# Kernel optimization log

Measured on AMD Instinct MI355X. Metric: run time of the kernel, lower is better.

## Reference

```python
import jax, jax.numpy as jnp
import numpy as np

N = 50000
E = 800000
IN_DIM = 128
HID = 128
OUT = 40


def setup_inputs() -> dict:
    key = jax.random.key(0)
    k1, k2, k3, k4, k5 = jax.random.split(key, 5)
    x = jax.random.normal(k1, (N, IN_DIM), dtype=jnp.float32)
    edge_index = jax.random.randint(k2, (2, E), 0, N, dtype=jnp.int64)
    # Glorot-ish init for GCNConv weights, zero bias (PyG default bias=True)
    W1 = jax.random.normal(k3, (IN_DIM, HID), dtype=jnp.float32) / np.sqrt(IN_DIM)
    b1 = jnp.zeros((HID,), dtype=jnp.float32)
    W2 = jax.random.normal(k4, (HID, OUT), dtype=jnp.float32) / np.sqrt(HID)
    b2 = jnp.zeros((OUT,), dtype=jnp.float32)
    return {"x": x, "edge_index": edge_index, "W1": W1, "b1": b1, "W2": W2, "b2": b2}


def _gcn_norm(edge_index, n_nodes):
    """Add self-loops and compute symmetric GCN normalization per edge.
    Returns (src, dst, norm) with len E + n_nodes."""
    loops = jnp.arange(n_nodes, dtype=edge_index.dtype)
    src = jnp.concatenate([edge_index[0], loops])
    dst = jnpp_concat = jnp.concatenate([edge_index[1], loops])
    dst = jnp.concatenate([edge_index[1], loops])
    deg = jax.ops.segment_sum(jnp.ones_like(dst, dtype=jnp.float32), dst,
                              num_segments=n_nodes)
    dinv = jnp.where(deg > 0, jax.lax.rsqrt(deg), 0.0)
    norm = dinv[src] * dinv[dst]  # [E + N]
    return src, dst, norm


def _gcn_conv(x, src, dst, norm, W, b, n_nodes):
    xw = x @ W                                  # [N, F_out] transform first
    msg = xw[src] * norm[:, None]               # gather + scale, [E+N, F_out]
    out = jax.ops.segment_sum(msg, dst, num_segments=n_nodes)  # scatter-add
    return out + b


def reference(x, edge_index, W1, b1, W2, b2):
    n = x.shape[0]
    src, dst, norm = _gcn_norm(edge_index, n)
    h = _gcn_conv(x, src, dst, norm, W1, b1, n)
    h = jax.nn.relu(h)
    # dropout is identity in eval mode (training=False)
    h = _gcn_conv(h, src, dst, norm, W2, b2, n)
    return jax.nn.softmax(h, axis=1)
```

## Files before the change

### kernel.cpp

```cpp
#include <hip/hip_runtime.h>
#include <hip/hip_fp16.h>

#define IN_DIM 128
#define HID    128
#define OUTC   40
#define CAP    64
#define LSTR   136
#define NBS    1024

typedef _Float16 f16x8 __attribute__((ext_vector_type(8)));
typedef _Float16 f16x4 __attribute__((ext_vector_type(4)));
typedef float    f32x4 __attribute__((ext_vector_type(4)));
typedef int      i32x4 __attribute__((ext_vector_type(4)));

__device__ __forceinline__ int permi(int d, int NP8) { return (d & 7) * NP8 + (d >> 3); }

__device__ __forceinline__ f16x8 cvt8(f32x4 lo, f32x4 hi) {
  f16x8 r;
  r[0] = (_Float16)lo[0]; r[1] = (_Float16)lo[1]; r[2] = (_Float16)lo[2]; r[3] = (_Float16)lo[3];
  r[4] = (_Float16)hi[0]; r[5] = (_Float16)hi[1]; r[6] = (_Float16)hi[2]; r[7] = (_Float16)hi[3];
  return r;
}

__global__ __launch_bounds__(256) void k_scatter(const int* __restrict__ edge, int* __restrict__ cnt,
                                                 unsigned short* __restrict__ col,
                                                 int E, int n, int NP8) {
  int b = blockIdx.x, tid = threadIdx.x;
  int g = b & 7;
  int E4 = E >> 2;
  auto proc = [&](int d, int s) {
    if ((d & 7) != g || (unsigned)d >= (unsigned)n || (unsigned)s >= (unsigned)n) return;
    int p   = g * NP8 + (d >> 3);
    int pos = atomicAdd(&cnt[p], 1);
    if (pos < CAP) col[(size_t)p * CAP + pos] = (unsigned short)s;
  };
  int j = b >> 3;
  int t = j * 256 + tid;
  const int gstride = (NBS >> 3) * 256;
  const i32x4* srcv = (const i32x4*)edge;
  const i32x4* dstv = (const i32x4*)&edge[E];
  for (int q = t; q < E4; q += gstride) {
    i32x4 dq = __builtin_nontemporal_load(&dstv[q]);
    i32x4 sq = __builtin_nontemporal_load(&srcv[q]);
    proc(dq[0], sq[0]); proc(dq[1], sq[1]); proc(dq[2], sq[2]); proc(dq[3], sq[3]);
  }
  if (b == 0) {
    for (int e = E4 * 4 + tid; e < E; e += 256) {
      int d  = edge[E + e];
      int sv = edge[e];
      if ((unsigned)d >= (unsigned)n || (unsigned)sv >= (unsigned)n) continue;
      int p   = (d & 7) * NP8 + (d >> 3);
      int pos = atomicAdd(&cnt[p], 1);
      if (pos < CAP) col[(size_t)p * CAP + pos] = (unsigned short)sv;
    }
  }
}

__global__ __launch_bounds__(256) void k_gemm1(const float* __restrict__ x, const float* __restrict__ W1,
                                               const int* __restrict__ cnt, __half* __restrict__ xws,
                                               int n, int NP8) {
  __shared__ _Float16 sW[128 * LSTR];
  int tid = threadIdx.x;
  int i0  = blockIdx.x * 64;

  {
    const f32x4* w4 = (const f32x4*)W1;
    for (int idx = tid; idx < 4096; idx += 256) {
      int kk = idx >> 5, nn4 = (idx & 31) * 4;
      f32x4 v = w4[idx];
      sW[(nn4 + 0) * LSTR + kk] = (_Float16)v[0];
      sW[(nn4 + 1) * LSTR + kk] = (_Float16)v[1];
      sW[(nn4 + 2) * LSTR + kk] = (_Float16)v[2];
      sW[(nn4 + 3) * LSTR + kk] = (_Float16)v[3];
    }
  }
  __syncthreads();

  int wv = tid >> 6, lane = tid & 63, m = lane & 15, quad = lane >> 4;
  int arow = i0 + 16 * wv + m;
  f16x8 a0, a1, a2, a3;
  if (arow < n) {
    const float* xr = &x[(size_t)arow * IN_DIM + quad * 8];
    f32x4 u0 = __builtin_nontemporal_load((const f32x4*)(xr));
    f32x4 u1 = __builtin_nontemporal_load((const f32x4*)(xr + 4));
    f32x4 u2 = __builtin_nontemporal_load((const f32x4*)(xr + 32));
    f32x4 u3 = __builtin_nontemporal_load((const f32x4*)(xr + 36));
    f32x4 u4 = __builtin_nontemporal_load((const f32x4*)(xr + 64));
    f32x4 u5 = __builtin_nontemporal_load((const f32x4*)(xr + 68));
    f32x4 u6 = __builtin_nontemporal_load((const f32x4*)(xr + 96));
    f32x4 u7 = __builtin_nontemporal_load((const f32x4*)(xr + 100));
    a0 = cvt8(u0, u1); a1 = cvt8(u2, u3); a2 = cvt8(u4, u5); a3 = cvt8(u6, u7);
  } else {
#pragma unroll
    for (int jj = 0; jj < 8; ++jj) {
      a0[jj] = (_Float16)0.f; a1[jj] = (_Float16)0.f; a2[jj] = (_Float16)0.f; a3[jj] = (_Float16)0.f;
    }
  }

  int base_row = i0 + 16 * wv + quad * 4;
  float dvr[4];
#pragma unroll
  for (int r = 0; r < 4; ++r) {
    int row = base_row + r;
    dvr[r] = (row < n) ? rsqrtf((float)(cnt[permi(row, NP8)] + 1)) : 0.f;
  }

#pragma unroll
  for (int t = 0; t < 8; ++t) {
    const _Float16* bx = &sW[(t * 16 + m) * LSTR + quad * 8];
    f16x8 bf0 = *(const f16x8*)(bx);
    f16x8 bf1 = *(const f16x8*)(bx + 32);
    f16x8 bf2 = *(const f16x8*)(bx + 64);
    f16x8 bf3 = *(const f16x8*)(bx + 96);
    f32x4 c = {0.f, 0.f, 0.f, 0.f};
    c = __builtin_amdgcn_mfma_f32_16x16x32_f16(a0, bf0, c, 0, 0, 0);
    c = __builtin_amdgcn_mfma_f32_16x16x32_f16(a1, bf1, c, 0, 0, 0);
    c = __builtin_amdgcn_mfma_f32_16x16x32_f16(a2, bf2, c, 0, 0, 0);
    c = __builtin_amdgcn_mfma_f32_16x16x32_f16(a3, bf3, c, 0, 0, 0);
    int colb = t * 16 + m;
#pragma unroll
    for (int r = 0; r < 4; ++r) {
      int row = base_row + r;
      if (row < n) xws[(size_t)row * HID + colb] = __float2half(c[r] * dvr[r]);
    }
  }
}

__global__ __launch_bounds__(256) void k_agg1(const uint2* __restrict__ xws2, const int* __restrict__ cnt,
                                              const unsigned short* __restrict__ col, const float* __restrict__ b1,
                                              uint2* __restrict__ hv, int n, int NP8, int nbHalf) {
  int bi = blockIdx.x, tid = threadIdx.x;
  int ph = 0;
  if (bi >= nbHalf) { ph = 1; bi -= nbHalf; }
  int sub = (tid >> 4) & 3;
  int f16i = tid & 15;
  int wid = bi * 16 + ((tid >> 6) << 2) + sub;
  if (wid >= n) return;
  int fo = ph * 16 + f16i;
  int p   = permi(wid, NP8);
  int deg = cnt[p];
  float dvd = rsqrtf((float)(deg + 1));
  uint2 sv = xws2[(size_t)wid * 32 + fo];
  float2 alo = __half22float2(*(__half2*)&sv.x);
  float2 ahi = __half22float2(*(__half2*)&sv.y);
  float ax = alo.x, ay = alo.y, az = ahi.x, aw = ahi.y;
  int end = min(deg, CAP);
  const unsigned short* cp = &col[(size_t)p * CAP];
  int e = 0;
  for (; e + 4 <= end; e += 4) {
    uint2 cw = *(const uint2*)&cp[e];
    int s0 = cw.x & 0xffff, s1 = cw.x >> 16;
    int s2 = cw.y & 0xffff, s3 = cw.y >> 16;
    uint2 v0 = xws2[(size_t)s0 * 32 + fo];
    uint2 v1 = xws2[(size_t)s1 * 32 + fo];
    uint2 v2 = xws2[(size_t)s2 * 32 + fo];
    uint2 v3 = xws2[(size_t)s3 * 32 + fo];
    float2 l0 = __half22float2(*(__half2*)&v0.x), h0 = __half22float2(*(__half2*)&v0.y);
    float2 l1 = __half22float2(*(__half2*)&v1.x), h1 = __half22float2(*(__half2*)&v1.y);
    float2 l2 = __half22float2(*(__half2*)&v2.x), h2 = __half22float2(*(__half2*)&v2.y);
    float2 l3 = __half22float2(*(__half2*)&v3.x), h3 = __half22float2(*(__half2*)&v3.y);
    ax += (l0.x + l1.x) + (l2.x + l3.x);
    ay += (l0.y + l1.y) + (l2.y + l3.y);
    az += (h0.x + h1.x) + (h2.x + h3.x);
    aw += (h0.y + h1.y) + (h2.y + h3.y);
  }
  for (; e < end; ++e) {
    uint2 v = xws2[(size_t)cp[e] * 32 + fo];
    float2 l = __half22float2(*(__half2*)&v.x), hh = __half22float2(*(__half2*)&v.y);
    ax += l.x; ay += l.y; az += hh.x; aw += hh.y;
  }
  float4 bb = ((const float4*)b1)[fo];
  __half2 o0 = __floats2half2_rn(fmaxf(ax * dvd + bb.x, 0.f), fmaxf(ay * dvd + bb.y, 0.f));
  __half2 o1 = __floats2half2_rn(fmaxf(az * dvd + bb.z, 0.f), fmaxf(aw * dvd + bb.w, 0.f));
  uint2 o; o.x = *(unsigned*)&o0; o.y = *(unsigned*)&o1;
  hv[(size_t)wid * 32 + fo] = o;
}

__global__ __launch_bounds__(256) void k_gemm2(const __half* __restrict__ h, const float* __restrict__ W2,
                                               const int* __restrict__ cnt, __half* __restrict__ out,
                                               int n, int NP8) {
  __shared__ _Float16 sW[48 * LSTR];
  __shared__ _Float16 sH[64 * LSTR];
  int tid = threadIdx.x;
  int i0  = blockIdx.x * 64;

  for (int idx = tid; idx < 8192; idx += 256) {
    int nn = idx & 63, kk = idx >> 6;
    if (nn < 48) sW[nn * LSTR + kk] = (nn < OUTC) ? (_Float16)W2[kk * OUTC + nn] : (_Float16)0.f;
  }
  {
    const uint4* src = (const uint4*)h;
    for (int idx = tid; idx < 1024; idx += 256) {
      int r = idx >> 4, c = idx & 15;
      int row = i0 + r;
      uint4 v = (row < n) ? src[(size_t)row * 16 + c] : make_uint4(0u, 0u, 0u, 0u);
      *(uint4*)&sH[r * LSTR + c * 8] = v;
    }
  }
  __syncthreads();

  int wv = tid >> 6, lane = tid & 63, m = lane & 15, quad = lane >> 4;
  const _Float16* axp = &sH[(16 * wv + m) * LSTR + quad * 8];
  f16x8 a0 = *(const f16x8*)(axp);
  f16x8 a1 = *(const f16x8*)(axp + 32);
  f16x8 a2 = *(const f16x8*)(axp + 64);
  f16x8 a3 = *(const f16x8*)(axp + 96);

  int base_row = i0 + 16 * wv + quad * 4;
  float dvr[4];
#pragma unroll
  for (int r = 0; r < 4; ++r) {
    int row = base_row + r;
    dvr[r] = (row < n) ? rsqrtf((float)(cnt[permi(row, NP8)] + 1)) : 0.f;
  }

#pragma unroll
  for (int t = 0; t < 3; ++t) {
    const _Float16* bx = &sW[(t * 16 + m) * LSTR + quad * 8];
    f16x8 bf0 = *(const f16x8*)(bx);
    f16x8 bf1 = *(const f16x8*)(bx + 32);
    f16x8 bf2 = *(const f16x8*)(bx + 64);
    f16x8 bf3 = *(const f16x8*)(bx + 96);
    f32x4 c = {0.f, 0.f, 0.f, 0.f};
    c = __builtin_amdgcn_mfma_f32_16x16x32_f16(a0, bf0, c, 0, 0, 0);
    c = __builtin_amdgcn_mfma_f32_16x16x32_f16(a1, bf1, c, 0, 0, 0);
    c = __builtin_amdgcn_mfma_f32_16x16x32_f16(a2, bf2, c, 0, 0, 0);
    c = __builtin_amdgcn_mfma_f32_16x16x32_f16(a3, bf3, c, 0, 0, 0);
    int colb = t * 16 + m;
    if (colb < OUTC) {
#pragma unroll
      for (int r = 0; r < 4; ++r) {
        int row = base_row + r;
        if (row < n) out[(size_t)row * OUTC + colb] = __float2half(c[r] * dvr[r]);
      }
    }
  }
}

__global__ __launch_bounds__(256) void k_agg2(const __half2* __restrict__ hw2, const int* __restrict__ cnt,
                                              const unsigned short* __restrict__ col, const float* __restrict__ b2,
                                              float* __restrict__ out, int n, int NP8) {
  int wpair = (blockIdx.x * 256 + threadIdx.x) >> 6;
  int lane  = threadIdx.x & 63;
  int half  = lane >> 5;
  int f     = lane & 31;
  int wid   = wpair * 2 + half;
  bool act  = (f < OUTC / 2) && (wid < n);
  int widc  = (wid < n) ? wid : 0;
  int li    = act ? f : 0;
  int p     = permi(widc, NP8);
  int deg   = (wid < n) ? cnt[p] : 0;
  float2 acc = act ? __half22float2(hw2[(size_t)widc * (OUTC / 2) + li]) : make_float2(0.f, 0.f);
  int end = min(deg, CAP);
  const unsigned short* cp = &col[(size_t)p * CAP];
  int e = 0;
  for (; e + 8 <= end; e += 8) {
    uint4 cw = *(const uint4*)&cp[e];
    int s0 = cw.x & 0xffff, s1 = cw.x >> 16, s2 = cw.y & 0xffff, s3 = cw.y >> 16;
    int s4 = cw.z & 0xffff, s5 = cw.z >> 16, s6 = cw.w & 0xffff, s7 = cw.w >> 16;
    if (act) {
      float2 v0 = __half22float2(hw2[(size_t)s0 * (OUTC / 2) + li]);
      float2 v1 = __half22float2(hw2[(size_t)s1 * (OUTC / 2) + li]);
      float2 v2 = __half22float2(hw2[(size_t)s2 * (OUTC / 2) + li]);
      float2 v3 = __half22float2(hw2[(size_t)s3 * (OUTC / 2) + li]);
      float2 v4 = __half22float2(hw2[(size_t)s4 * (OUTC / 2) + li]);
      float2 v5 = __half22float2(hw2[(size_t)s5 * (OUTC / 2) + li]);
      float2 v6 = __half22float2(hw2[(size_t)s6 * (OUTC / 2) + li]);
      float2 v7 = __half22float2(hw2[(size_t)s7 * (OUTC / 2) + li]);
      acc.x += (v0.x + v1.x) + (v2.x + v3.x) + ((v4.x + v5.x) + (v6.x + v7.x));
      acc.y += (v0.y + v1.y) + (v2.y + v3.y) + ((v4.y + v5.y) + (v6.y + v7.y));
    }
  }
  for (; e < end; ++e) {
    int s = cp[e];
    if (act) {
      float2 v = __half22float2(hw2[(size_t)s * (OUTC / 2) + li]);
      acc.x += v.x; acc.y += v.y;
    }
  }
  float dvd = rsqrtf((float)(deg + 1));
  float2 bb = act ? ((const float2*)b2)[li] : make_float2(0.f, 0.f);
  float lx = act ? acc.x * dvd + bb.x : -1e30f;
  float ly = act ? acc.y * dvd + bb.y : -1e30f;
  float m = fmaxf(lx, ly);
#pragma unroll
  for (int o = 16; o > 0; o >>= 1) m = fmaxf(m, __shfl_xor(m, o, 32));
  float ex = act ? __expf(lx - m) : 0.f;
  float ey = act ? __expf(ly - m) : 0.f;
  float sum = ex + ey;
#pragma unroll
  for (int o = 16; o > 0; o >>= 1) sum += __shfl_xor(sum, o, 32);
  if (act) {
    float inv = 1.f / sum;
    ((float2*)out)[(size_t)wid * (OUTC / 2) + li] = make_float2(ex * inv, ey * inv);
  }
}


extern "C" void kernel_launch(void* const* d_in, const int* in_sizes, int n_in,
                              void* d_out, int out_size, void* d_ws, size_t ws_size,
                              hipStream_t stream) {
  const float* x    = (const float*)d_in[0];
  const int*   edge = (const int*)d_in[1];
  const float* W1   = (const float*)d_in[2];
  const float* b1   = (const float*)d_in[3];
  const float* W2   = (const float*)d_in[4];
  const float* b2   = (const float*)d_in[5];
  float* out = (float*)d_out;

  int N   = in_sizes[0] / IN_DIM;
  int E   = in_sizes[1] / 2;
  int NP8 = (N + 7) / 8;
  int NP  = NP8 * 8;

  char* ws = (char*)d_ws;
  size_t off = 0;
  auto carve = [&](size_t bytes) { char* p = ws + off; off = (off + bytes + 255) & ~(size_t)255; return p; };
  int*            cnt = (int*)carve((size_t)NP * 4);
  unsigned short* col = (unsigned short*)carve((size_t)NP * CAP * 2);
  __half*         xws = (__half*)carve((size_t)N * HID * 2);
  __half*         h   = (__half*)carve((size_t)N * HID * 2);
  __half*         hw  = xws;

  (void)hipMemsetAsync(cnt, 0, (size_t)NP * 4, stream);

  int nT     = (N + 63) / 64;
  int nbHalf = (N + 15) / 16;
  int nbA2   = ((N + 1) / 2 * 64 + 255) / 256;

  k_scatter<<<NBS, 256, 0, stream>>>(edge, cnt, col, E, N, NP8);
  k_gemm1<<<nT, 256, 0, stream>>>(x, W1, cnt, xws, N, NP8);
  k_agg1<<<2 * nbHalf, 256, 0, stream>>>((const uint2*)xws, cnt, col, b1, (uint2*)h, N, NP8, nbHalf);
  k_gemm2<<<nT, 256, 0, stream>>>(h, W2, cnt, hw, N, NP8);
  k_agg2<<<nbA2, 256, 0, stream>>>((const __half2*)hw, cnt, col, b2, out, N, NP8);
}
```

Measured before the change: 217.8 us.

## Store XW in feature-sliced layout and aggregate one 32-feature slice per block

GEMM1 now writes its fp16 output as four 32-column slices, each laid out contiguously per node ([slice][node][32]). Each aggregation block handles a single slice, with 8 threads per node, so the gathered working set per pass is a quarter of the feature matrix and should stay resident in L2/cache. In exchange each gather moves only 64 bytes per neighbour, and GEMM1 now issues strided scalar half stores.

```diff
diff --git a/kernel.cpp b/kernel.cpp
--- a/kernel.cpp
+++ b/kernel.cpp
@@ -118,32 +118,31 @@
     c = __builtin_amdgcn_mfma_f32_16x16x32_f16(a2, bf2, c, 0, 0, 0);
     c = __builtin_amdgcn_mfma_f32_16x16x32_f16(a3, bf3, c, 0, 0, 0);
     int colb = t * 16 + m;
+    int slice = colb >> 5, jj = colb & 31;
 #pragma unroll
     for (int r = 0; r < 4; ++r) {
       int row = base_row + r;
-      if (row < n) xws[(size_t)row * HID + colb] = __float2half(c[r] * dvr[r]);
-    }
-  }
-}
-
-__global__ __launch_bounds__(256) void k_agg1(const uint2* __restrict__ xws2, const int* __restrict__ cnt,
+      if (row < n) xws[((size_t)slice * n + row) * 32 + jj] = __float2half(c[r] * dvr[r]);
+    }
+  }
+}
+
+__global__ __launch_bounds__(256) void k_agg1(const uint2* __restrict__ xs2, const int* __restrict__ cnt,
                                               const unsigned short* __restrict__ col, const float* __restrict__ b1,
-                                              uint2* __restrict__ hv, int n, int NP8, int nbHalf) {
-  int bi = blockIdx.x, tid = threadIdx.x;
-  int ph = 0;
-  if (bi >= nbHalf) { ph = 1; bi -= nbHalf; }
-  int sub = (tid >> 4) & 3;
-  int f16i = tid & 15;
-  int wid = bi * 16 + ((tid >> 6) << 2) + sub;
-  if (wid >= n) return;
-  int fo = ph * 16 + f16i;
-  int p   = permi(wid, NP8);
+                                              __half* __restrict__ h, int n, int NP8) {
+  int b     = blockIdx.x;
+  int slice = b & 3;
+  int node  = (b >> 2) * 32 + (threadIdx.x >> 3);
+  int ln    = threadIdx.x & 7;
+  if (node >= n) return;
+  int p   = permi(node, NP8);
   int deg = cnt[p];
   float dvd = rsqrtf((float)(deg + 1));
-  uint2 sv = xws2[(size_t)wid * 32 + fo];
-  float2 alo = __half22float2(*(__half2*)&sv.x);
-  float2 ahi = __half22float2(*(__half2*)&sv.y);
-  float ax = alo.x, ay = alo.y, az = ahi.x, aw = ahi.y;
+  const size_t sbase = (size_t)slice * n * 8;
+  uint2 sv = xs2[sbase + (size_t)node * 8 + ln];
+  float2 slo = __half22float2(*(__half2*)&sv.x);
+  float2 shi = __half22float2(*(__half2*)&sv.y);
+  float ax = slo.x, ay = slo.y, az = shi.x, aw = shi.y;
   int end = min(deg, CAP);
   const unsigned short* cp = &col[(size_t)p * CAP];
   int e = 0;
@@ -151,10 +150,10 @@
     uint2 cw = *(const uint2*)&cp[e];
     int s0 = cw.x & 0xffff, s1 = cw.x >> 16;
     int s2 = cw.y & 0xffff, s3 = cw.y >> 16;
-    uint2 v0 = xws2[(size_t)s0 * 32 + fo];
-    uint2 v1 = xws2[(size_t)s1 * 32 + fo];
-    uint2 v2 = xws2[(size_t)s2 * 32 + fo];
-    uint2 v3 = xws2[(size_t)s3 * 32 + fo];
+    uint2 v0 = xs2[sbase + (size_t)s0 * 8 + ln];
+    uint2 v1 = xs2[sbase + (size_t)s1 * 8 + ln];
+    uint2 v2 = xs2[sbase + (size_t)s2 * 8 + ln];
+    uint2 v3 = xs2[sbase + (size_t)s3 * 8 + ln];
     float2 l0 = __half22float2(*(__half2*)&v0.x), h0 = __half22float2(*(__half2*)&v0.y);
     float2 l1 = __half22float2(*(__half2*)&v1.x), h1 = __half22float2(*(__half2*)&v1.y);
     float2 l2 = __half22float2(*(__half2*)&v2.x), h2 = __half22float2(*(__half2*)&v2.y);
@@ -165,15 +164,17 @@
     aw += (h0.y + h1.y) + (h2.y + h3.y);
   }
   for (; e < end; ++e) {
-    uint2 v = xws2[(size_t)cp[e] * 32 + fo];
+    uint2 v = xs2[sbase + (size_t)cp[e] * 8 + ln];
     float2 l = __half22float2(*(__half2*)&v.x), hh = __half22float2(*(__half2*)&v.y);
     ax += l.x; ay += l.y; az += hh.x; aw += hh.y;
   }
-  float4 bb = ((const float4*)b1)[fo];
-  __half2 o0 = __floats2half2_rn(fmaxf(ax * dvd + bb.x, 0.f), fmaxf(ay * dvd + bb.y, 0.f));
-  __half2 o1 = __floats2half2_rn(fmaxf(az * dvd + bb.z, 0.f), fmaxf(aw * dvd + bb.w, 0.f));
-  uint2 o; o.x = *(unsigned*)&o0; o.y = *(unsigned*)&o1;
-  hv[(size_t)wid * 32 + fo] = o;
+  float4 bb = ((const float4*)b1)[slice * 8 + ln];
+  f16x4 o;
+  o[0] = (_Float16)fmaxf(ax * dvd + bb.x, 0.f);
+  o[1] = (_Float16)fmaxf(ay * dvd + bb.y, 0.f);
+  o[2] = (_Float16)fmaxf(az * dvd + bb.z, 0.f);
+  o[3] = (_Float16)fmaxf(aw * dvd + bb.w, 0.f);
+  *(f16x4*)&h[(size_t)node * HID + slice * 32 + ln * 4] = o;
 }
 
 __global__ __launch_bounds__(256) void k_gemm2(const __half* __restrict__ h, const float* __restrict__ W2,
@@ -324,13 +325,13 @@
 
   (void)hipMemsetAsync(cnt, 0, (size_t)NP * 4, stream);
 
-  int nT     = (N + 63) / 64;
-  int nbHalf = (N + 15) / 16;
-  int nbA2   = ((N + 1) / 2 * 64 + 255) / 256;
+  int nT   = (N + 63) / 64;
+  int nbA1 = 4 * ((N + 31) / 32);
+  int nbA2 = ((N + 1) / 2 * 64 + 255) / 256;
 
   k_scatter<<<NBS, 256, 0, stream>>>(edge, cnt, col, E, N, NP8);
   k_gemm1<<<nT, 256, 0, stream>>>(x, W1, cnt, xws, N, NP8);
-  k_agg1<<<2 * nbHalf, 256, 0, stream>>>((const uint2*)xws, cnt, col, b1, (uint2*)h, N, NP8, nbHalf);
+  k_agg1<<<nbA1, 256, 0, stream>>>((const uint2*)xws, cnt, col, b1, h, N, NP8);
   k_gemm2<<<nT, 256, 0, stream>>>(h, W2, cnt, hw, N, NP8);
   k_agg2<<<nbA2, 256, 0, stream>>>((const __half2*)hw, cnt, col, b2, out, N, NP8);
 }
```

Result: no change. 221.2 us (+1.6%).

## Remap agg1 to 32 lanes per node, pad layer-2 rows to 64, double scatter blocks

Applied to the files above, without the earlier changes.

k_agg1 now gives each node 32 lanes that cover all 128 features, replacing the two-phase split where separate blocks each handled half the features. Every neighbor row is therefore fetched as one contiguous 256-byte segment, and each node's degree and adjacency list are read once instead of twice. The layer-2 transformed features are stored with a 64-half row pitch instead of 40, so gathered rows line up with 128-byte boundaries, at the cost of extra footprint and write bandwidth. The scatter kernel's block count is also doubled.

```diff
diff --git a/kernel.cpp b/kernel.cpp
--- a/kernel.cpp
+++ b/kernel.cpp
@@ -4,9 +4,10 @@
 #define IN_DIM 128
 #define HID    128
 #define OUTC   40
+#define HWP    64
 #define CAP    64
 #define LSTR   136
-#define NBS    1024
+#define NBS    2048
 
 typedef _Float16 f16x8 __attribute__((ext_vector_type(8)));
 typedef _Float16 f16x4 __attribute__((ext_vector_type(4)));
@@ -128,22 +129,19 @@
 
 __global__ __launch_bounds__(256) void k_agg1(const uint2* __restrict__ xws2, const int* __restrict__ cnt,
                                               const unsigned short* __restrict__ col, const float* __restrict__ b1,
-                                              uint2* __restrict__ hv, int n, int NP8, int nbHalf) {
-  int bi = blockIdx.x, tid = threadIdx.x;
-  int ph = 0;
-  if (bi >= nbHalf) { ph = 1; bi -= nbHalf; }
-  int sub = (tid >> 4) & 3;
-  int f16i = tid & 15;
-  int wid = bi * 16 + ((tid >> 6) << 2) + sub;
+                                              uint2* __restrict__ hv, int n, int NP8) {
+  int wvid = (blockIdx.x * 256 + threadIdx.x) >> 6;
+  int lane = threadIdx.x & 63;
+  int half = lane >> 5;
+  int f    = lane & 31;
+  int wid  = wvid * 2 + half;
   if (wid >= n) return;
-  int fo = ph * 16 + f16i;
-  int p   = permi(wid, NP8);
-  int deg = cnt[p];
-  float dvd = rsqrtf((float)(deg + 1));
-  uint2 sv = xws2[(size_t)wid * 32 + fo];
+  uint2 sv = xws2[(size_t)wid * 32 + f];
   float2 alo = __half22float2(*(__half2*)&sv.x);
   float2 ahi = __half22float2(*(__half2*)&sv.y);
   float ax = alo.x, ay = alo.y, az = ahi.x, aw = ahi.y;
+  int p   = permi(wid, NP8);
+  int deg = cnt[p];
   int end = min(deg, CAP);
   const unsigned short* cp = &col[(size_t)p * CAP];
   int e = 0;
@@ -151,10 +149,10 @@
     uint2 cw = *(const uint2*)&cp[e];
     int s0 = cw.x & 0xffff, s1 = cw.x >> 16;
     int s2 = cw.y & 0xffff, s3 = cw.y >> 16;
-    uint2 v0 = xws2[(size_t)s0 * 32 + fo];
-    uint2 v1 = xws2[(size_t)s1 * 32 + fo];
-    uint2 v2 = xws2[(size_t)s2 * 32 + fo];
-    uint2 v3 = xws2[(size_t)s3 * 32 + fo];
+    uint2 v0 = xws2[(size_t)s0 * 32 + f];
+    uint2 v1 = xws2[(size_t)s1 * 32 + f];
+    uint2 v2 = xws2[(size_t)s2 * 32 + f];
+    uint2 v3 = xws2[(size_t)s3 * 32 + f];
     float2 l0 = __half22float2(*(__half2*)&v0.x), h0 = __half22float2(*(__half2*)&v0.y);
     float2 l1 = __half22float2(*(__half2*)&v1.x), h1 = __half22float2(*(__half2*)&v1.y);
     float2 l2 = __half22float2(*(__half2*)&v2.x), h2 = __half22float2(*(__half2*)&v2.y);
@@ -165,15 +163,16 @@
     aw += (h0.y + h1.y) + (h2.y + h3.y);
   }
   for (; e < end; ++e) {
-    uint2 v = xws2[(size_t)cp[e] * 32 + fo];
+    uint2 v = xws2[(size_t)cp[e] * 32 + f];
     float2 l = __half22float2(*(__half2*)&v.x), hh = __half22float2(*(__half2*)&v.y);
     ax += l.x; ay += l.y; az += hh.x; aw += hh.y;
   }
-  float4 bb = ((const float4*)b1)[fo];
-  __half2 o0 = __floats2half2_rn(fmaxf(ax * dvd + bb.x, 0.f), fmaxf(ay * dvd + bb.y, 0.f));
-  __half2 o1 = __floats2half2_rn(fmaxf(az * dvd + bb.z, 0.f), fmaxf(aw * dvd + bb.w, 0.f));
+  float dv = rsqrtf((float)(deg + 1));
+  float4 bb = ((const float4*)b1)[f];
+  __half2 o0 = __floats2half2_rn(fmaxf(ax * dv + bb.x, 0.f), fmaxf(ay * dv + bb.y, 0.f));
+  __half2 o1 = __floats2half2_rn(fmaxf(az * dv + bb.z, 0.f), fmaxf(aw * dv + bb.w, 0.f));
   uint2 o; o.x = *(unsigned*)&o0; o.y = *(unsigned*)&o1;
-  hv[(size_t)wid * 32 + fo] = o;
+  hv[(size_t)wid * 32 + f] = o;
 }
 
 __global__ __launch_bounds__(256) void k_gemm2(const __half* __restrict__ h, const float* __restrict__ W2,
@@ -231,7 +230,7 @@
 #pragma unroll
       for (int r = 0; r < 4; ++r) {
         int row = base_row + r;
-        if (row < n) out[(size_t)row * OUTC + colb] = __float2half(c[r] * dvr[r]);
+        if (row < n) out[(size_t)row * HWP + colb] = __float2half(c[r] * dvr[r]);
       }
     }
   }
@@ -250,7 +249,7 @@
   int li    = act ? f : 0;
   int p     = permi(widc, NP8);
   int deg   = (wid < n) ? cnt[p] : 0;
-  float2 acc = act ? __half22float2(hw2[(size_t)widc * (OUTC / 2) + li]) : make_float2(0.f, 0.f);
+  float2 acc = act ? __half22float2(hw2[(size_t)widc * (HWP / 2) + li]) : make_float2(0.f, 0.f);
   int end = min(deg, CAP);
   const unsigned short* cp = &col[(size_t)p * CAP];
   int e = 0;
@@ -259,14 +258,14 @@
     int s0 = cw.x & 0xffff, s1 = cw.x >> 16, s2 = cw.y & 0xffff, s3 = cw.y >> 16;
     int s4 = cw.z & 0xffff, s5 = cw.z >> 16, s6 = cw.w & 0xffff, s7 = cw.w >> 16;
     if (act) {
-      float2 v0 = __half22float2(hw2[(size_t)s0 * (OUTC / 2) + li]);
-      float2 v1 = __half22float2(hw2[(size_t)s1 * (OUTC / 2) + li]);
-      float2 v2 = __half22float2(hw2[(size_t)s2 * (OUTC / 2) + li]);
-      float2 v3 = __half22float2(hw2[(size_t)s3 * (OUTC / 2) + li]);
-      float2 v4 = __half22float2(hw2[(size_t)s4 * (OUTC / 2) + li]);
-      float2 v5 = __half22float2(hw2[(size_t)s5 * (OUTC / 2) + li]);
-      float2 v6 = __half22float2(hw2[(size_t)s6 * (OUTC / 2) + li]);
-      float2 v7 = __half22float2(hw2[(size_t)s7 * (OUTC / 2) + li]);
+      float2 v0 = __half22float2(hw2[(size_t)s0 * (HWP / 2) + li]);
+      float2 v1 = __half22float2(hw2[(size_t)s1 * (HWP / 2) + li]);
+      float2 v2 = __half22float2(hw2[(size_t)s2 * (HWP / 2) + li]);
+      float2 v3 = __half22float2(hw2[(size_t)s3 * (HWP / 2) + li]);
+      float2 v4 = __half22float2(hw2[(size_t)s4 * (HWP / 2) + li]);
+      float2 v5 = __half22float2(hw2[(size_t)s5 * (HWP / 2) + li]);
+      float2 v6 = __half22float2(hw2[(size_t)s6 * (HWP / 2) + li]);
+      float2 v7 = __half22float2(hw2[(size_t)s7 * (HWP / 2) + li]);
       acc.x += (v0.x + v1.x) + (v2.x + v3.x) + ((v4.x + v5.x) + (v6.x + v7.x));
       acc.y += (v0.y + v1.y) + (v2.y + v3.y) + ((v4.y + v5.y) + (v6.y + v7.y));
     }
@@ -274,7 +273,7 @@
   for (; e < end; ++e) {
     int s = cp[e];
     if (act) {
-      float2 v = __half22float2(hw2[(size_t)s * (OUTC / 2) + li]);
+      float2 v = __half22float2(hw2[(size_t)s * (HWP / 2) + li]);
       acc.x += v.x; acc.y += v.y;
     }
   }
@@ -324,13 +323,12 @@
 
   (void)hipMemsetAsync(cnt, 0, (size_t)NP * 4, stream);
 
-  int nT     = (N + 63) / 64;
-  int nbHalf = (N + 15) / 16;
-  int nbA2   = ((N + 1) / 2 * 64 + 255) / 256;
+  int nT   = (N + 63) / 64;
+  int nbA  = ((N + 1) / 2 * 64 + 255) / 256;
 
   k_scatter<<<NBS, 256, 0, stream>>>(edge, cnt, col, E, N, NP8);
   k_gemm1<<<nT, 256, 0, stream>>>(x, W1, cnt, xws, N, NP8);
-  k_agg1<<<2 * nbHalf, 256, 0, stream>>>((const uint2*)xws, cnt, col, b1, (uint2*)h, N, NP8, nbHalf);
+  k_agg1<<<nbA, 256, 0, stream>>>((const uint2*)xws, cnt, col, b1, (uint2*)h, N, NP8);
   k_gemm2<<<nT, 256, 0, stream>>>(h, W2, cnt, hw, N, NP8);
-  k_agg2<<<nbA2, 256, 0, stream>>>((const __half2*)hw, cnt, col, b2, out, N, NP8);
-}
+  k_agg2<<<nbA, 256, 0, stream>>>((const __half2*)hw, cnt, col, b2, out, N, NP8);
+}
```

Result: no change. 218.4 us (+0.3%).
